# Kernel tuning notes

Measured on AMD Instinct MI355X. Metric: run time of the kernel, lower is better.

## Reference

```python
import jax, jax.numpy as jnp
import numpy as np

RADIUS = 0.1
NSAMPLE = 32


def _ball_query(new_xyz, xyz, radius, nsample):
    # new_xyz: (B, S, 3), xyz: (B, N, 3) -> idx (B, S, nsample) int32
    N = xyz.shape[1]
    d2 = jnp.sum((new_xyz[:, :, None, :] - xyz[:, None, :, :]) ** 2, axis=-1)  # (B,S,N)
    mask = d2 < radius * radius
    cand = jnp.where(mask, jnp.arange(N, dtype=jnp.int32)[None, None, :], N)
    cand = jnp.sort(cand, axis=-1)[:, :, :nsample]  # first nsample in-ball indices
    first = cand[:, :, :1]
    first = jnp.where(first == N, 0, first)  # empty ball -> index 0 (CUDA semantics)
    return jnp.where(cand == N, first, cand).astype(jnp.int32)


def _group(features, idx):
    # features: (B, C, N), idx: (B, S, K) -> (B, C, S, K)
    return jax.vmap(lambda f, i: f[:, i])(features, idx)


def setup_inputs() -> dict:
    key = jax.random.key(0)
    k1, k2, k3, k4 = jax.random.split(key, 4)
    B, N, S, C = 4, 16384, 2048, 64
    xyz = jax.random.uniform(k1, (B, N, 3), dtype=jnp.float32)
    new_xyz = jax.random.uniform(k2, (B, S, 3), dtype=jnp.float32)
    features = jax.random.normal(k3, (B, C, N), dtype=jnp.float32)
    fps_idx = jax.random.randint(k4, (B, S), 0, N, dtype=jnp.int32)
    return {"xyz": xyz, "new_xyz": new_xyz, "features": features, "fps_idx": fps_idx}


def reference(xyz, new_xyz, features, fps_idx):
    idx = _ball_query(new_xyz, xyz, RADIUS, NSAMPLE)          # (B,S,nsample)
    idx = jnp.concatenate([fps_idx[:, :, None], idx], axis=2)  # (B,S,nsample+1)
    xyz_t = jnp.transpose(xyz, (0, 2, 1))                      # (B,3,N)
    raw_grouped_xyz = _group(xyz_t, idx)                       # (B,3,S,K)
    grouped_xyz = raw_grouped_xyz - jnp.transpose(new_xyz, (0, 2, 1))[..., None]
    grouped_features = _group(features, idx)                   # (B,C,S,K)
    return jnp.concatenate([raw_grouped_xyz, grouped_xyz, grouped_features], axis=1)
```

## Files before the change

### kernel.cpp

```cpp
#include <hip/hip_runtime.h>

#define BB 4
#define NN 16384
#define SS 2048
#define CC 64
#define NS 32
#define KK 33
#define OC 70
#define SCH 4
#define GT 512
#define NC 10
#define NCELL 1000
#define CCAP 64
#define HCAP 224
#define HSEG 112
#define RPAD 0.100001f

__device__ __forceinline__ float sq_nofma(float v) {
  float r = v * v;
  asm volatile("" : "+v"(r));
  return r;
}

__device__ __forceinline__ int cell1(float x) {
  int c = (int)(x * 10.0f);
  return c < 0 ? 0 : (c > 9 ? 9 : c);
}
__device__ __forceinline__ int cell3(float x, float y, float z) {
  return (cell1(z) * NC + cell1(y)) * NC + cell1(x);
}

__device__ __forceinline__ void ball_query_wave(
    const float* __restrict__ xb, float qx, float qy, float qz, int lane,
    int* out) {
  const float R2 = 0.01f;
  int cnt = 0;
  int firstIdx = 0;
  for (int base = 0; base < NN; base += 256) {
    float px[4], py[4], pz[4];
#pragma unroll
    for (int j = 0; j < 4; ++j) {
      int n = base + j * 64 + lane;
      const float* p = xb + n * 3;
      px[j] = p[0]; py[j] = p[1]; pz[j] = p[2];
    }
#pragma unroll
    for (int j = 0; j < 4; ++j) {
      float dx = px[j] - qx, dy = py[j] - qy, dz = pz[j] - qz;
      float d2 = sq_nofma(dx) + sq_nofma(dy);
      asm volatile("" : "+v"(d2));
      d2 = d2 + sq_nofma(dz);
      bool m = d2 < R2;
      unsigned long long bal = __ballot(m);
      if (cnt == 0 && bal) firstIdx = base + j * 64 + __builtin_ctzll(bal);
      int pos = cnt + (int)__popcll(bal & ((1ull << lane) - 1ull));
      if (m && pos < NS) out[pos] = base + j * 64 + lane;
      cnt += (int)__popcll(bal);
    }
    if (cnt >= NS) break;
  }
  if (cnt < NS) {
    int pad = (cnt == 0) ? 0 : firstIdx;
    if (lane >= cnt && lane < NS) out[lane] = pad;
  }
}

__global__ __launch_bounds__(256) void qg_tr_build(
    const float* __restrict__ xyz, const float* __restrict__ feat,
    float* __restrict__ featT, int* __restrict__ cnt, int* __restrict__ ovf,
    float4* __restrict__ ptsc) {
  __shared__ float tile[32 * 260];
  const int bid = (int)blockIdx.x;
  const int tid = (int)threadIdx.x;
  const int b = bid >> 7;
  const int rest = bid & 127;
  const int n0 = (rest >> 1) << 8;
  const int cc = rest & 1;
  const int c0 = cc << 5;
  const int wv = tid >> 6, lane = tid & 63;

  if (cc == 0) {
    const int n = n0 + tid;
    const float* p = xyz + ((size_t)b * NN + n) * 3;
    float x = p[0], y = p[1], z = p[2];
    int cell = cell3(x, y, z);
    int pos = atomicAdd(&cnt[(b << 10) + cell], 1);
    if (pos < CCAP) {
      ptsc[((((size_t)b << 10) + cell) << 6) + pos] =
          make_float4(x, y, z, __int_as_float(n));
    } else {
      atomicOr(&ovf[b], 1);
    }
  }

  const float* fb = feat + ((size_t)b * CC + c0) * NN + n0;
#pragma unroll
  for (int rr = 0; rr < 8; ++rr) {
    int c = rr * 4 + wv;
    float4 v = *(const float4*)(fb + (size_t)c * NN + 4 * lane);
    *(float4*)&tile[c * 260 + 4 * lane] = v;
  }
  __syncthreads();
  const int c4 = lane & 7, m = lane >> 3;
  float4* oT = (float4*)(featT + ((size_t)b * NN + n0) * CC);
#pragma unroll
  for (int it = 0; it < 8; ++it) {
    int n = it * 32 + wv * 8 + m;
    float4 v;
    v.x = tile[(4 * c4 + 0) * 260 + n];
    v.y = tile[(4 * c4 + 1) * 260 + n];
    v.z = tile[(4 * c4 + 2) * 260 + n];
    v.w = tile[(4 * c4 + 3) * 260 + n];
    oT[(size_t)n * (CC / 4) + (c0 >> 2) + c4] = v;
  }
}

__global__ __launch_bounds__(GT) void qg_main(
    const float* __restrict__ xyz, const float* __restrict__ nxyz,
    const float4* __restrict__ ptsc, const int* __restrict__ cnt,
    const int* __restrict__ ovf, const float* __restrict__ featT,
    const int* __restrict__ fps, float* __restrict__ out) {
  __shared__ float sf[CC][SCH * KK + 1];
  __shared__ int sidx[SCH * KK];
  __shared__ int hitbuf[SCH][HCAP];
  __shared__ int hcnt_s[SCH][2];
  const int tid = (int)threadIdx.x;
  const int raw = (int)blockIdx.x;
  const int blk = (raw & 7) * (BB * SS / SCH / 8)
                  + (raw >> 3);
  const int b = blk >> 9;
  const int s0 = (blk & 511) * SCH;
  const int wv = tid >> 6, lane = tid & 63;
  const int wq = wv >> 1;
  const int h = wv & 1;
  const int q = b * SS + s0 + wq;
  const float R2 = 0.01f;
  const float qx = nxyz[q * 3 + 0];
  const float qy = nxyz[q * 3 + 1];
  const float qz = nxyz[q * 3 + 2];
  int* hb = hitbuf[wq];
  int* qout = &sidx[wq * KK];
  const bool bad = ovf[b] != 0;

  if (!bad) {
    int lox = max(0, (int)floorf((qx - RPAD) * 10.f));
    int hix = min(9, (int)floorf((qx + RPAD) * 10.f));
    int loy = max(0, (int)floorf((qy - RPAD) * 10.f));
    int hiy = min(9, (int)floorf((qy + RPAD) * 10.f));
    int loz = max(0, (int)floorf((qz - RPAD) * 10.f));
    int hiz = min(9, (int)floorf((qz + RPAD) * 10.f));
    const int ncx = hix - lox + 1, ncy = hiy - loy + 1, ncz = hiz - loz + 1;
    const int ncell = ncx * ncy * ncz;

    const int* cntb = cnt + (b << 10);
    int cell_l = 0, cnt_l = 0;
    if (lane < ncell) {
      int iz = lane / (ncx * ncy);
      int r = lane - iz * ncx * ncy;
      int iy = r / ncx, ix = r - iy * ncx;
      cell_l = ((loz + iz) * NC + (loy + iy)) * NC + (lox + ix);
      cnt_l = cntb[cell_l];
    }

    const float4* pcb = ptsc + ((size_t)b << 16);
    const unsigned long long lt = (1ull << lane) - 1ull;
    const int slot = lane & 31;
    const int half = lane >> 5;
    const int npair = (ncell + 1) >> 1;
    const int hp2 = (npair + 1) >> 1;
    const int p_beg = h * hp2;
    const int p_end = min(npair, p_beg + hp2);
    const int wbase = h * HSEG;
    int hcnt = 0;

#define PAIRLOAD(pp)                                                       \
  ({                                                                       \
    int pc_ = ((pp) < p_end) ? (pp) : p_beg;                               \
    int ca_ = __shfl(cell_l, 2 * pc_, 64);                                 \
    int cb_ = __shfl(cell_l, 2 * pc_ + 1, 64);                             \
    pcb[(((half ? cb_ : ca_)) << 6) + slot];                               \
  })

    float4 v0 = PAIRLOAD(p_beg);
    float4 v1 = PAIRLOAD(p_beg + 1);
    for (int p = p_beg; p < p_end; ++p) {
      float4 v = v0;
      v0 = v1;
      v1 = PAIRLOAD(p + 2);
      int m0 = __shfl(cnt_l, 2 * p, 64);
      int m1 = __shfl(cnt_l, 2 * p + 1, 64);
      int m = half ? m1 : m0;
      {
        float dx = v.x - qx, dy = v.y - qy, dz = v.z - qz;
        float d2 = sq_nofma(dx) + sq_nofma(dy);
        asm volatile("" : "+v"(d2));
        d2 = d2 + sq_nofma(dz);
        bool hit = (slot < m) && (d2 < R2);
        unsigned long long bal = __ballot(hit);
        if (hit) {
          int pos = hcnt + (int)__popcll(bal & lt);
          if (pos < HSEG) hb[wbase + pos] = __float_as_int(v.w);
        }
        hcnt += (int)__popcll(bal);
      }
      if (m0 > 32 || m1 > 32) {
        int ca = __shfl(cell_l, 2 * p, 64);
        int cb = __shfl(cell_l, 2 * p + 1, 64);
        float4 w = pcb[(((half ? cb : ca)) << 6) + 32 + slot];
        float dx = w.x - qx, dy = w.y - qy, dz = w.z - qz;
        float d2 = sq_nofma(dx) + sq_nofma(dy);
        asm volatile("" : "+v"(d2));
        d2 = d2 + sq_nofma(dz);
        bool hit = (32 + slot < m) && (d2 < R2);
        unsigned long long bal = __ballot(hit);
        if (hit) {
          int pos = hcnt + (int)__popcll(bal & lt);
          if (pos < HSEG) hb[wbase + pos] = __float_as_int(w.w);
        }
        hcnt += (int)__popcll(bal);
      }
    }
#undef PAIRLOAD
    if (lane == 0) hcnt_s[wq][h] = hcnt;
  }
  __syncthreads();

  if (h == 0) {
    if (bad) {
      ball_query_wave(xyz + (size_t)b * NN * 3, qx, qy, qz, lane, qout + 1);
    } else {
      const int MA = hcnt_s[wq][0], MB = hcnt_s[wq][1];
      if (MA > HSEG || MB > HSEG) {
        ball_query_wave(xyz + (size_t)b * NN * 3, qx, qy, qz, lane, qout + 1);
      } else {
        for (int t = lane; t < MB; t += 64) hb[MA + t] = hb[HSEG + t];
        asm volatile("s_waitcnt lgkmcnt(0)" ::: "memory");
        const int M = MA + MB;
        int minv = 0x7fffffff;
        for (int i = lane; i < M; i += 64) {
          int hh = hb[i];
          minv = min(minv, hh);
          int rank = 0;
          for (int j = 0; j < M; ++j) rank += (hb[j] < hh) ? 1 : 0;
          if (rank < NS) qout[1 + rank] = hh;
        }
        if (M < NS) {
#pragma unroll
          for (int d = 1; d < 64; d <<= 1)
            minv = min(minv, __shfl_xor(minv, d, 64));
          int pad = (M == 0) ? 0 : minv;
          if (lane >= M && lane < NS) qout[1 + lane] = pad;
        }
      }
    }
    if (lane == 0) qout[0] = fps[q];
  }
  __syncthreads();

  const size_t cstr = (size_t)SS * KK;
  const float4* fT4 = (const float4*)(featT + (size_t)b * NN * CC);
  {
    const int e = tid & 15;
    const int g = tid >> 4;
    const bool has4 = (g + 128) < SCH * KK;
    int n0_ = sidx[g];
    int n1_ = sidx[g + 32];
    int n2_ = sidx[g + 64];
    int n3_ = sidx[g + 96];
    int n4_ = has4 ? sidx[g + 128] : 0;
    float4 w0 = fT4[(size_t)n0_ * (CC / 4) + e];
    float4 w1 = fT4[(size_t)n1_ * (CC / 4) + e];
    float4 w2 = fT4[(size_t)n2_ * (CC / 4) + e];
    float4 w3 = fT4[(size_t)n3_ * (CC / 4) + e];
    float4 w4 = has4 ? fT4[(size_t)n4_ * (CC / 4) + e]
                     : make_float4(0.f, 0.f, 0.f, 0.f);
    sf[4 * e + 0][g] = w0.x;
    sf[4 * e + 1][g] = w0.y;
    sf[4 * e + 2][g] = w0.z;
    sf[4 * e + 3][g] = w0.w;
    sf[4 * e + 0][g + 32] = w1.x;
    sf[4 * e + 1][g + 32] = w1.y;
    sf[4 * e + 2][g + 32] = w1.z;
    sf[4 * e + 3][g + 32] = w1.w;
    sf[4 * e + 0][g + 64] = w2.x;
    sf[4 * e + 1][g + 64] = w2.y;
    sf[4 * e + 2][g + 64] = w2.z;
    sf[4 * e + 3][g + 64] = w2.w;
    sf[4 * e + 0][g + 96] = w3.x;
    sf[4 * e + 1][g + 96] = w3.y;
    sf[4 * e + 2][g + 96] = w3.z;
    sf[4 * e + 3][g + 96] = w3.w;
    if (has4) {
      sf[4 * e + 0][g + 128] = w4.x;
      sf[4 * e + 1][g + 128] = w4.y;
      sf[4 * e + 2][g + 128] = w4.z;
      sf[4 * e + 3][g + 128] = w4.w;
    }
  }

  if (tid < SCH * KK) {
    int s4 = tid / KK;
    int n = sidx[tid];
    const float* p = xyz + ((size_t)b * NN + n) * 3;
    float x = p[0], y = p[1], z = p[2];
    int qq = b * SS + s0 + s4;
    float cx = nxyz[qq * 3 + 0], cy = nxyz[qq * 3 + 1], cz = nxyz[qq * 3 + 2];
    size_t obase = ((size_t)(b * OC) * SS + s0) * KK + tid;
    out[obase + 0 * cstr] = x;
    out[obase + 1 * cstr] = y;
    out[obase + 2 * cstr] = z;
    out[obase + 3 * cstr] = x - cx;
    out[obase + 4 * cstr] = y - cy;
    out[obase + 5 * cstr] = z - cz;
  }
  __syncthreads();

  size_t fbase = ((size_t)(b * OC + 6) * SS + s0) * KK;
  for (int idx = tid; idx < CC * SCH * KK; idx += GT) {
    int c = idx / (SCH * KK);
    int j = idx - c * (SCH * KK);
    out[fbase + (size_t)c * cstr + j] = sf[c][j];
  }
}

__global__ __launch_bounds__(256) void qg_ballq(
    const float* __restrict__ xyz, const float* __restrict__ nxyz,
    int* __restrict__ wsidx) {
  int q = (int)((blockIdx.x * blockDim.x + threadIdx.x) >> 6);
  int lane = (int)(threadIdx.x & 63);
  int b = q / SS;
  const float* xb = xyz + (size_t)b * NN * 3;
  ball_query_wave(xb, nxyz[q * 3], nxyz[q * 3 + 1], nxyz[q * 3 + 2], lane,
                  wsidx + (size_t)q * NS);
}

__global__ __launch_bounds__(256) void qg_gather(
    const float* __restrict__ xyz, const float* __restrict__ nxyz,
    const float* __restrict__ feat, const int* __restrict__ fps,
    const int* __restrict__ wsidx, float* __restrict__ out) {
  unsigned t = blockIdx.x * 256u + threadIdx.x;
  const unsigned TOT = (unsigned)BB * OC * SS * KK;
  if (t >= TOT) return;
  unsigned k = t % KK;
  unsigned r = t / KK;
  unsigned s = r % SS;
  r /= SS;
  unsigned c = r % OC;
  unsigned b = r / OC;
  unsigned q = b * SS + s;
  int n = (k == 0) ? fps[q] : wsidx[(size_t)q * NS + (k - 1)];
  float v;
  if (c < 6) {
    unsigned cc = (c < 3) ? c : c - 3;
    v = xyz[((size_t)b * NN + (unsigned)n) * 3 + cc];
    if (c >= 3) v -= nxyz[q * 3 + cc];
  } else {
    v = feat[((size_t)b * CC + (c - 6)) * NN + (unsigned)n];
  }
  out[t] = v;
}

__global__ __launch_bounds__(256) void qg_fused(
    const float* __restrict__ xyz, const float* __restrict__ nxyz,
    const float* __restrict__ feat, const int* __restrict__ fps,
    float* __restrict__ out) {
  __shared__ int sidx[4][KK];
  int wv = (int)(threadIdx.x >> 6), lane = (int)(threadIdx.x & 63);
  int q = (int)blockIdx.x * 4 + wv;
  int b = q / SS, s = q % SS;
  const float* xb = xyz + (size_t)b * NN * 3;
  ball_query_wave(xb, nxyz[q * 3], nxyz[q * 3 + 1], nxyz[q * 3 + 2], lane,
                  &sidx[wv][1]);
  if (lane == 0) sidx[wv][0] = fps[q];
  __syncthreads();
  for (int f = lane; f < OC * KK; f += 64) {
    int c = f / KK, k = f - c * KK;
    int n = sidx[wv][k];
    float v;
    if (c < 6) {
      int cc = (c < 3) ? c : c - 3;
      v = xb[n * 3 + cc];
      if (c >= 3) v -= nxyz[q * 3 + cc];
    } else {
      v = feat[((size_t)b * CC + (c - 6)) * NN + n];
    }
    out[((size_t)((size_t)b * OC + c) * SS + s) * KK + k] = v;
  }
}

extern "C" void kernel_launch(void* const* d_in, const int* in_sizes, int n_in,
                              void* d_out, int out_size, void* d_ws, size_t ws_size,
                              hipStream_t stream) {
  const float* xyz  = (const float*)d_in[0];
  const float* nxyz = (const float*)d_in[1];
  const float* feat = (const float*)d_in[2];
  const int*   fps  = (const int*)d_in[3];
  float* out = (float*)d_out;

  const size_t ptsc_b  = (size_t)BB * 1024 * CCAP * sizeof(float4);
  const size_t cnt_b   = 32768;
  const size_t featT_b = (size_t)BB * NN * CC * sizeof(float);
  const size_t grid_need = ptsc_b + cnt_b + featT_b;

  const size_t idx_b = (size_t)BB * SS * NS * sizeof(int);

  if (ws_size >= grid_need) {
    char* w = (char*)d_ws;
    float4* ptsc  = (float4*)w;                      w += ptsc_b;
    int*    cnt   = (int*)w;                         w += cnt_b;
    float*  featT = (float*)w;
    int*    ovf   = cnt + BB * 1024;
    hipMemsetAsync(cnt, 0, cnt_b, stream);
    qg_tr_build<<<512, 256, 0, stream>>>(xyz, feat, featT, cnt, ovf, ptsc);
    qg_main<<<BB * (SS / SCH), GT, 0, stream>>>(xyz, nxyz, ptsc, cnt, ovf,
                                                featT, fps, out);
  } else if (ws_size >= idx_b) {
    int* wsidx = (int*)d_ws;
    qg_ballq<<<(BB * SS) / 4, 256, 0, stream>>>(xyz, nxyz, wsidx);
    unsigned tot = (unsigned)BB * OC * SS * KK;
    qg_gather<<<(tot + 255u) / 256u, 256, 0, stream>>>(xyz, nxyz, feat, fps,
                                                       wsidx, out);
  } else {
    qg_fused<<<(BB * SS) / 4, 256, 0, stream>>>(xyz, nxyz, feat, fps, out);
  }
}
```

Before: 49.68 us.

## Assign one wave per query and process eight queries per block

Each block now handles eight queries, with one wave per query, instead of four queries with two waves each splitting the cell pairs. This drops the cross-wave hit-count exchange, the merge of the two half buffers and one block barrier. The feature gather runs as two serial halves that reuse the same shared tile, so half as many blocks are launched. The risk is a longer serial ball-query scan per wave and an extra barrier inside the gather loop.

```diff
diff --git a/kernel.cpp b/kernel.cpp
--- a/kernel.cpp
+++ b/kernel.cpp
@@ -7,13 +7,12 @@
 #define NS 32
 #define KK 33
 #define OC 70
-#define SCH 4
+#define SCH 8
 #define GT 512
 #define NC 10
 #define NCELL 1000
 #define CCAP 64
-#define HCAP 224
-#define HSEG 112
+#define HCAP 128
 #define RPAD 0.100001f
 
 __device__ __forceinline__ float sq_nofma(float v) {
@@ -120,29 +119,27 @@
     const float4* __restrict__ ptsc, const int* __restrict__ cnt,
     const int* __restrict__ ovf, const float* __restrict__ featT,
     const int* __restrict__ fps, float* __restrict__ out) {
-  __shared__ float sf[CC][SCH * KK + 1];
+  __shared__ float sf[CC][4 * KK + 1];
   __shared__ int sidx[SCH * KK];
-  __shared__ int hitbuf[SCH][HCAP];
-  __shared__ int hcnt_s[SCH][2];
+  __shared__ int hitbuf[8][HCAP];
   const int tid = (int)threadIdx.x;
   const int raw = (int)blockIdx.x;
-  const int blk = (raw & 7) * (BB * SS / SCH / 8)
-                  + (raw >> 3);
-  const int b = blk >> 9;
-  const int s0 = (blk & 511) * SCH;
+  const int blk = (raw & 7) * 128 + (raw >> 3);
+  const int b = blk >> 8;
+  const int s0 = (blk & 255) * SCH;
   const int wv = tid >> 6, lane = tid & 63;
-  const int wq = wv >> 1;
-  const int h = wv & 1;
-  const int q = b * SS + s0 + wq;
+  const int q = b * SS + s0 + wv;
   const float R2 = 0.01f;
   const float qx = nxyz[q * 3 + 0];
   const float qy = nxyz[q * 3 + 1];
   const float qz = nxyz[q * 3 + 2];
-  int* hb = hitbuf[wq];
-  int* qout = &sidx[wq * KK];
+  int* hb = hitbuf[wv];
+  int* qout = &sidx[wv * KK];
   const bool bad = ovf[b] != 0;
 
-  if (!bad) {
+  if (bad) {
+    ball_query_wave(xyz + (size_t)b * NN * 3, qx, qy, qz, lane, qout + 1);
+  } else {
     int lox = max(0, (int)floorf((qx - RPAD) * 10.f));
     int hix = min(9, (int)floorf((qx + RPAD) * 10.f));
     int loy = max(0, (int)floorf((qy - RPAD) * 10.f));
@@ -167,23 +164,19 @@
     const int slot = lane & 31;
     const int half = lane >> 5;
     const int npair = (ncell + 1) >> 1;
-    const int hp2 = (npair + 1) >> 1;
-    const int p_beg = h * hp2;
-    const int p_end = min(npair, p_beg + hp2);
-    const int wbase = h * HSEG;
     int hcnt = 0;
 
 #define PAIRLOAD(pp)                                                       \
   ({                                                                       \
-    int pc_ = ((pp) < p_end) ? (pp) : p_beg;                               \
+    int pc_ = ((pp) < npair) ? (pp) : 0;                                   \
     int ca_ = __shfl(cell_l, 2 * pc_, 64);                                 \
     int cb_ = __shfl(cell_l, 2 * pc_ + 1, 64);                             \
     pcb[(((half ? cb_ : ca_)) << 6) + slot];                               \
   })
 
-    float4 v0 = PAIRLOAD(p_beg);
-    float4 v1 = PAIRLOAD(p_beg + 1);
-    for (int p = p_beg; p < p_end; ++p) {
+    float4 v0 = PAIRLOAD(0);
+    float4 v1 = PAIRLOAD(1);
+    for (int p = 0; p < npair; ++p) {
       float4 v = v0;
       v0 = v1;
       v1 = PAIRLOAD(p + 2);
@@ -199,7 +192,7 @@
         unsigned long long bal = __ballot(hit);
         if (hit) {
           int pos = hcnt + (int)__popcll(bal & lt);
-          if (pos < HSEG) hb[wbase + pos] = __float_as_int(v.w);
+          if (pos < HCAP) hb[pos] = __float_as_int(v.w);
         }
         hcnt += (int)__popcll(bal);
       }
@@ -215,111 +208,107 @@
         unsigned long long bal = __ballot(hit);
         if (hit) {
           int pos = hcnt + (int)__popcll(bal & lt);
-          if (pos < HSEG) hb[wbase + pos] = __float_as_int(w.w);
+          if (pos < HCAP) hb[pos] = __float_as_int(w.w);
         }
         hcnt += (int)__popcll(bal);
       }
     }
 #undef PAIRLOAD
-    if (lane == 0) hcnt_s[wq][h] = hcnt;
-  }
-  __syncthreads();
-
-  if (h == 0) {
-    if (bad) {
+
+    asm volatile("s_waitcnt lgkmcnt(0)" ::: "memory");
+    const int M = hcnt;
+    if (M > HCAP) {
       ball_query_wave(xyz + (size_t)b * NN * 3, qx, qy, qz, lane, qout + 1);
     } else {
-      const int MA = hcnt_s[wq][0], MB = hcnt_s[wq][1];
-      if (MA > HSEG || MB > HSEG) {
-        ball_query_wave(xyz + (size_t)b * NN * 3, qx, qy, qz, lane, qout + 1);
-      } else {
-        for (int t = lane; t < MB; t += 64) hb[MA + t] = hb[HSEG + t];
-        asm volatile("s_waitcnt lgkmcnt(0)" ::: "memory");
-        const int M = MA + MB;
-        int minv = 0x7fffffff;
-        for (int i = lane; i < M; i += 64) {
-          int hh = hb[i];
-          minv = min(minv, hh);
-          int rank = 0;
-          for (int j = 0; j < M; ++j) rank += (hb[j] < hh) ? 1 : 0;
-          if (rank < NS) qout[1 + rank] = hh;
-        }
-        if (M < NS) {
-#pragma unroll
-          for (int d = 1; d < 64; d <<= 1)
-            minv = min(minv, __shfl_xor(minv, d, 64));
-          int pad = (M == 0) ? 0 : minv;
-          if (lane >= M && lane < NS) qout[1 + lane] = pad;
-        }
+      int minv = 0x7fffffff;
+      for (int i = lane; i < M; i += 64) {
+        int hh = hb[i];
+        minv = min(minv, hh);
+        int rank = 0;
+        for (int j = 0; j < M; ++j) rank += (hb[j] < hh) ? 1 : 0;
+        if (rank < NS) qout[1 + rank] = hh;
       }
-    }
-    if (lane == 0) qout[0] = fps[q];
-  }
+      if (M < NS) {
+#pragma unroll
+        for (int d = 1; d < 64; d <<= 1)
+          minv = min(minv, __shfl_xor(minv, d, 64));
+        int pad = (M == 0) ? 0 : minv;
+        if (lane >= M && lane < NS) qout[1 + lane] = pad;
+      }
+    }
+  }
+  if (lane == 0) qout[0] = fps[q];
   __syncthreads();
 
   const size_t cstr = (size_t)SS * KK;
   const float4* fT4 = (const float4*)(featT + (size_t)b * NN * CC);
-  {
-    const int e = tid & 15;
-    const int g = tid >> 4;
-    const bool has4 = (g + 128) < SCH * KK;
-    int n0_ = sidx[g];
-    int n1_ = sidx[g + 32];
-    int n2_ = sidx[g + 64];
-    int n3_ = sidx[g + 96];
-    int n4_ = has4 ? sidx[g + 128] : 0;
-    float4 w0 = fT4[(size_t)n0_ * (CC / 4) + e];
-    float4 w1 = fT4[(size_t)n1_ * (CC / 4) + e];
-    float4 w2 = fT4[(size_t)n2_ * (CC / 4) + e];
-    float4 w3 = fT4[(size_t)n3_ * (CC / 4) + e];
-    float4 w4 = has4 ? fT4[(size_t)n4_ * (CC / 4) + e]
-                     : make_float4(0.f, 0.f, 0.f, 0.f);
-    sf[4 * e + 0][g] = w0.x;
-    sf[4 * e + 1][g] = w0.y;
-    sf[4 * e + 2][g] = w0.z;
-    sf[4 * e + 3][g] = w0.w;
-    sf[4 * e + 0][g + 32] = w1.x;
-    sf[4 * e + 1][g + 32] = w1.y;
-    sf[4 * e + 2][g + 32] = w1.z;
-    sf[4 * e + 3][g + 32] = w1.w;
-    sf[4 * e + 0][g + 64] = w2.x;
-    sf[4 * e + 1][g + 64] = w2.y;
-    sf[4 * e + 2][g + 64] = w2.z;
-    sf[4 * e + 3][g + 64] = w2.w;
-    sf[4 * e + 0][g + 96] = w3.x;
-    sf[4 * e + 1][g + 96] = w3.y;
-    sf[4 * e + 2][g + 96] = w3.z;
-    sf[4 * e + 3][g + 96] = w3.w;
-    if (has4) {
-      sf[4 * e + 0][g + 128] = w4.x;
-      sf[4 * e + 1][g + 128] = w4.y;
-      sf[4 * e + 2][g + 128] = w4.z;
-      sf[4 * e + 3][g + 128] = w4.w;
-    }
-  }
-
-  if (tid < SCH * KK) {
-    int s4 = tid / KK;
-    int n = sidx[tid];
-    const float* p = xyz + ((size_t)b * NN + n) * 3;
-    float x = p[0], y = p[1], z = p[2];
-    int qq = b * SS + s0 + s4;
-    float cx = nxyz[qq * 3 + 0], cy = nxyz[qq * 3 + 1], cz = nxyz[qq * 3 + 2];
-    size_t obase = ((size_t)(b * OC) * SS + s0) * KK + tid;
-    out[obase + 0 * cstr] = x;
-    out[obase + 1 * cstr] = y;
-    out[obase + 2 * cstr] = z;
-    out[obase + 3 * cstr] = x - cx;
-    out[obase + 4 * cstr] = y - cy;
-    out[obase + 5 * cstr] = z - cz;
-  }
-  __syncthreads();
-
-  size_t fbase = ((size_t)(b * OC + 6) * SS + s0) * KK;
-  for (int idx = tid; idx < CC * SCH * KK; idx += GT) {
-    int c = idx / (SCH * KK);
-    int j = idx - c * (SCH * KK);
-    out[fbase + (size_t)c * cstr + j] = sf[c][j];
+#pragma unroll
+  for (int hf = 0; hf < 2; ++hf) {
+    const int base = hf * 4 * KK;
+    {
+      const int e = tid & 15;
+      const int g = tid >> 4;
+      const bool has4 = (g + 128) < 4 * KK;
+      int n0_ = sidx[base + g];
+      int n1_ = sidx[base + g + 32];
+      int n2_ = sidx[base + g + 64];
+      int n3_ = sidx[base + g + 96];
+      int n4_ = has4 ? sidx[base + g + 128] : 0;
+      float4 w0 = fT4[(size_t)n0_ * (CC / 4) + e];
+      float4 w1 = fT4[(size_t)n1_ * (CC / 4) + e];
+      float4 w2 = fT4[(size_t)n2_ * (CC / 4) + e];
+      float4 w3 = fT4[(size_t)n3_ * (CC / 4) + e];
+      float4 w4 = has4 ? fT4[(size_t)n4_ * (CC / 4) + e]
+                       : make_float4(0.f, 0.f, 0.f, 0.f);
+      sf[4 * e + 0][g] = w0.x;
+      sf[4 * e + 1][g] = w0.y;
+      sf[4 * e + 2][g] = w0.z;
+      sf[4 * e + 3][g] = w0.w;
+      sf[4 * e + 0][g + 32] = w1.x;
+      sf[4 * e + 1][g + 32] = w1.y;
+      sf[4 * e + 2][g + 32] = w1.z;
+      sf[4 * e + 3][g + 32] = w1.w;
+      sf[4 * e + 0][g + 64] = w2.x;
+      sf[4 * e + 1][g + 64] = w2.y;
+      sf[4 * e + 2][g + 64] = w2.z;
+      sf[4 * e + 3][g + 64] = w2.w;
+      sf[4 * e + 0][g + 96] = w3.x;
+      sf[4 * e + 1][g + 96] = w3.y;
+      sf[4 * e + 2][g + 96] = w3.z;
+      sf[4 * e + 3][g + 96] = w3.w;
+      if (has4) {
+        sf[4 * e + 0][g + 128] = w4.x;
+        sf[4 * e + 1][g + 128] = w4.y;
+        sf[4 * e + 2][g + 128] = w4.z;
+        sf[4 * e + 3][g + 128] = w4.w;
+      }
+    }
+
+    if (tid < 4 * KK) {
+      int s4 = tid / KK;
+      int n = sidx[base + tid];
+      const float* p = xyz + ((size_t)b * NN + n) * 3;
+      float x = p[0], y = p[1], z = p[2];
+      int qq = b * SS + s0 + hf * 4 + s4;
+      float cx = nxyz[qq * 3 + 0], cy = nxyz[qq * 3 + 1],
+            cz = nxyz[qq * 3 + 2];
+      size_t obase = ((size_t)(b * OC) * SS + s0 + hf * 4) * KK + tid;
+      out[obase + 0 * cstr] = x;
+      out[obase + 1 * cstr] = y;
+      out[obase + 2 * cstr] = z;
+      out[obase + 3 * cstr] = x - cx;
+      out[obase + 4 * cstr] = y - cy;
+      out[obase + 5 * cstr] = z - cz;
+    }
+    __syncthreads();
+
+    size_t fbase = ((size_t)(b * OC + 6) * SS + s0 + hf * 4) * KK;
+    for (int idx = tid; idx < CC * 4 * KK; idx += GT) {
+      int c = idx / (4 * KK);
+      int j = idx - c * (4 * KK);
+      out[fbase + (size_t)c * cstr + j] = sf[c][j];
+    }
+    __syncthreads();
   }
 }
 
```

Result: no change. 49.33 us (-0.7%).
